# Kernel tuning notes

Hardware: AMD Instinct MI355X
Metric: run time of the kernel (lower is better)

## Reference

```python
import jax, jax.numpy as jnp
import numpy as np

B, T, D_IN, D_OUT, H = 4, 2048, 1024, 1024, 16
HD = D_OUT // H  # head_dim = 64


def setup_inputs() -> dict:
    key = jax.random.key(0)
    ks = jax.random.split(key, 6)
    s_in = 1.0 / np.sqrt(D_IN)
    s_out = 1.0 / np.sqrt(D_OUT)
    return {
        "x": jax.random.normal(ks[0], (B, T, D_IN), dtype=jnp.float32),
        "W_query": jax.random.uniform(ks[1], (D_IN, D_OUT), jnp.float32, -s_in, s_in),
        "W_key": jax.random.uniform(ks[2], (D_IN, D_OUT), jnp.float32, -s_in, s_in),
        "W_value": jax.random.uniform(ks[3], (D_IN, D_OUT), jnp.float32, -s_in, s_in),
        "W_out": jax.random.uniform(ks[4], (D_OUT, D_OUT), jnp.float32, -s_out, s_out),
        "b_out": jax.random.uniform(ks[5], (D_OUT,), jnp.float32, -s_out, s_out),
    }


def reference(x, W_query, W_key, W_value, W_out, b_out):
    # x: [B, T, D_IN]
    q = (x @ W_query).reshape(B, T, H, HD).transpose(0, 2, 1, 3)  # [B,H,T,HD]
    k = (x @ W_key).reshape(B, T, H, HD).transpose(0, 2, 1, 3)
    v = (x @ W_value).reshape(B, T, H, HD).transpose(0, 2, 1, 3)
    scores = jnp.einsum("bhqd,bhkd->bhqk", q, k)  # [B,H,T,T]
    causal = jnp.triu(jnp.ones((T, T), dtype=bool), k=1)
    scores = jnp.where(causal, -jnp.inf, scores)
    weights = jax.nn.softmax(scores / jnp.sqrt(jnp.float32(HD)), axis=-1)
    ctx = jnp.einsum("bhqk,bhkd->bhqd", weights, v)  # [B,H,T,HD]
    ctx = ctx.transpose(0, 2, 1, 3).reshape(B, T, D_OUT)
    return ctx @ W_out + b_out
```

## Files before the change

### kernel.cpp

```cpp
#include <hip/hip_runtime.h>
#include <math.h>

#define Bb   4
#define Tt   2048
#define DIN  1024
#define DOUT 1024
#define NH   16
#define HD   64
#define BT   (Bb * Tt)

typedef __attribute__((ext_vector_type(8))) short bf16x8;
typedef __attribute__((ext_vector_type(4))) float f32x4;
typedef __attribute__((ext_vector_type(4))) short short4v;

__device__ __forceinline__ short f2bf(float f) {
  union { float f; unsigned u; } v; v.f = f;
  unsigned r = v.u + 0x7FFFu + ((v.u >> 16) & 1u);
  return (short)(r >> 16);
}

__device__ __forceinline__ unsigned pkbf(float a, float b) {
  unsigned r;
  asm("v_cvt_pk_bf16_f32 %0, %1, %2" : "=v"(r) : "v"(a), "v"(b));
  return r;
}

#define MFMA16(a, b, c) __builtin_amdgcn_mfma_f32_16x16x32_bf16((a), (b), (c), 0, 0, 0)

__device__ __forceinline__ void gload16(const short* g, short* l) {
  __builtin_amdgcn_global_load_lds(
      (const __attribute__((address_space(1))) void*)g,
      (__attribute__((address_space(3))) void*)l, 16, 0, 0);
}

__global__ __launch_bounds__(256) void cvt_x(const float* __restrict__ x,
                                             short* __restrict__ xb) {
  const int i = (blockIdx.x * 256 + threadIdx.x) * 4;
  float4 v = *(const float4*)(x + i);
  uint2 o;
  o.x = pkbf(v.x, v.y);
  o.y = pkbf(v.z, v.w);
  *(uint2*)(xb + i) = o;
}

__global__ __launch_bounds__(256) void cvt_wt(
    const float* __restrict__ W0, const float* __restrict__ W1,
    const float* __restrict__ W2, const float* __restrict__ W3,
    short* __restrict__ O0, short* __restrict__ O1,
    short* __restrict__ O2, short* __restrict__ O3) {
  const float* W = blockIdx.z == 0 ? W0 : blockIdx.z == 1 ? W1
                 : blockIdx.z == 2 ? W2 : W3;
  short* O = blockIdx.z == 0 ? O0 : blockIdx.z == 1 ? O1
           : blockIdx.z == 2 ? O2 : O3;
  __shared__ short t[64][65];
  const int n0 = blockIdx.x * 64, k0 = blockIdx.y * 64;
  const int tid = threadIdx.x;
#pragma unroll
  for (int i = 0; i < 16; ++i) {
    const int e = tid + 256 * i;
    const int k = e >> 6, n = e & 63;
    t[n][k] = f2bf(W[(size_t)(k0 + k) * DOUT + n0 + n]);
  }
  __syncthreads();
#pragma unroll
  for (int i = 0; i < 16; ++i) {
    const int e = tid + 256 * i;
    const int n = e >> 6, k = e & 63;
    O[(size_t)(n0 + n) * DIN + k0 + k] = t[n][k];
  }
}

template <bool QKV, bool F32OUT, bool BIAS>
__global__ __launch_bounds__(256) void gemm_bf16(
    const short* __restrict__ A, const short* __restrict__ Bt0,
    const float* __restrict__ bias, void* __restrict__ Cout,
    int M, int N, int K, float qsc) {
  constexpr int BM = 128, BN = 128, BK = 64;
  __shared__ __align__(16) short Asm[BM][BK];
  __shared__ __align__(16) short Bsm[BN][BK];

  const short* Bt = Bt0;
  short* Cb16 = (short*)Cout;
  float oscale = 1.0f;
  if (QKV) {
    const int z = blockIdx.z;
    Bt += (size_t)z * N * K;
    Cb16 += (size_t)z * M * N;
    if (z == 0) oscale = qsc;
  }

  const int tid = threadIdx.x;
  const int wid = tid >> 6, lane = tid & 63;
  const int lhi = lane >> 4, llo = lane & 15;
  const int bm = blockIdx.x * BM, bn = blockIdx.y * BN;
  const int wr = (wid >> 1) * 64, wc = (wid & 1) * 64;

  const int srow = lane >> 3;
  const int sca = ((lane & 7) ^ srow) * 8;

  f32x4 acc[4][4];
#pragma unroll
  for (int i = 0; i < 4; ++i)
#pragma unroll
    for (int j = 0; j < 4; ++j)
#pragma unroll
      for (int r = 0; r < 4; ++r) acc[i][j][r] = 0.0f;

  for (int k0 = 0; k0 < K; k0 += BK) {
    __syncthreads();
#pragma unroll
    for (int iss = 0; iss < 4; ++iss) {
      const int ra = wid * 32 + iss * 8 + srow;
      gload16(A + (size_t)(bm + ra) * K + k0 + sca, &Asm[wid * 32 + iss * 8][0]);
      gload16(Bt + (size_t)(bn + ra) * K + k0 + sca, &Bsm[wid * 32 + iss * 8][0]);
    }
    __syncthreads();

#pragma unroll
    for (int ks = 0; ks < 2; ++ks) {
      bf16x8 af[4], bfr[4];
#pragma unroll
      for (int i = 0; i < 4; ++i) {
        const int row = wr + i * 16 + llo;
        af[i] = *(const bf16x8*)&Asm[row][((ks * 4 + lhi) ^ (row & 7)) * 8];
      }
#pragma unroll
      for (int j = 0; j < 4; ++j) {
        const int row = wc + j * 16 + llo;
        bfr[j] = *(const bf16x8*)&Bsm[row][((ks * 4 + lhi) ^ (row & 7)) * 8];
      }
      __builtin_amdgcn_s_setprio(1);
#pragma unroll
      for (int i = 0; i < 4; ++i)
#pragma unroll
        for (int j = 0; j < 4; ++j)
          acc[i][j] = MFMA16(af[i], bfr[j], acc[i][j]);
      __builtin_amdgcn_s_setprio(0);
    }
  }

#pragma unroll
  for (int i = 0; i < 4; ++i)
#pragma unroll
    for (int j = 0; j < 4; ++j)
#pragma unroll
      for (int r = 0; r < 4; ++r) {
        const int row = bm + wr + i * 16 + lhi * 4 + r;
        const int col = bn + wc + j * 16 + llo;
        float v = acc[i][j][r] * oscale;
        if (BIAS) v += bias[col];
        if (F32OUT)
          ((float*)Cout)[(size_t)row * N + col] = v;
        else
          Cb16[(size_t)row * N + col] = f2bf(v);
      }
}

__global__ __launch_bounds__(512, 2) void attn_bf16(
    const short* __restrict__ Q, const short* __restrict__ K,
    const short* __restrict__ Vt_g, short* __restrict__ Ctx) {
  constexpr int LDK = 72;
  constexpr int LDV = 72;
  constexpr int LDP = 72;
  __shared__ __align__(16) short Ks[2][64][LDK];
  __shared__ __align__(16) short Vt[2][64][LDV];
  __shared__ __align__(16) short Ps[8][32][LDP];

  const int bid = blockIdx.x;
  const int qt = 7 - (bid >> 6);
  const int bh = bid & 63;
  const int b = bh >> 4, h = bh & 15;
  const int tid = threadIdx.x;
  const int wid = tid >> 6, lane = tid & 63;
  const int lhi = lane >> 4, llo = lane & 15;

  const size_t base_bt = (size_t)b * Tt;
  const int headoff = h * HD;
  const int q0 = qt * 256 + wid * 32;

  bf16x8 qf[2][2];
#pragma unroll
  for (int rb = 0; rb < 2; ++rb)
#pragma unroll
    for (int kf = 0; kf < 2; ++kf)
      qf[rb][kf] = *(const bf16x8*)&Q[(base_bt + q0 + rb * 16 + llo) * DOUT +
                                      headoff + kf * 32 + lhi * 8];

  float m_r[2] = {-1e30f, -1e30f}, l_r[2] = {0.0f, 0.0f};
  f32x4 oa[2][4];
#pragma unroll
  for (int rb = 0; rb < 2; ++rb)
#pragma unroll
    for (int j = 0; j < 4; ++j)
#pragma unroll
      for (int r = 0; r < 4; ++r) oa[rb][j][r] = 0.0f;

  const int skv = tid >> 3;
  const int sd0 = (tid & 7) * 8;

  const int ktmax = qt * 4 + 3;

  const short* kgp = K + (base_bt + skv) * DOUT + headoff + sd0;
  const short* vgp = Vt_g + (size_t)(headoff + skv) * BT + base_bt + sd0;

  {
    bf16x8 kreg = *(const bf16x8*)kgp;
    bf16x8 vreg = *(const bf16x8*)vgp;
    *(bf16x8*)&Ks[0][skv][sd0] = kreg;
    *(bf16x8*)&Vt[0][skv][sd0] = vreg;
    kgp += 64 * DOUT;
    vgp += 64;
  }
  __syncthreads();

  for (int kt = 0; kt <= ktmax; ++kt) {
    const int cur = kt & 1;

    bf16x8 kreg, vreg;
    const bool haveNext = kt < ktmax;
    if (haveNext) {
      kreg = *(const bf16x8*)kgp;
      vreg = *(const bf16x8*)vgp;
      kgp += 64 * DOUT;
      vgp += 64;
    }

    if (kt * 64 <= q0 + 31) {
      bf16x8 kf0[4], kf1[4];
#pragma unroll
      for (int j = 0; j < 4; ++j) {
        kf0[j] = *(const bf16x8*)&Ks[cur][j * 16 + llo][lhi * 8];
        kf1[j] = *(const bf16x8*)&Ks[cur][j * 16 + llo][32 + lhi * 8];
      }

#pragma unroll
      for (int rb = 0; rb < 2; ++rb) {
        f32x4 s[4];
        __builtin_amdgcn_s_setprio(1);
#pragma unroll
        for (int j = 0; j < 4; ++j) {
#pragma unroll
          for (int r = 0; r < 4; ++r) s[j][r] = 0.0f;
          s[j] = MFMA16(kf0[j], qf[rb][0], s[j]);
          s[j] = MFMA16(kf1[j], qf[rb][1], s[j]);
        }
        __builtin_amdgcn_s_setprio(0);
        if (kt * 64 + 63 > q0 + rb * 16) {
          const int kvrel = kt * 64 + lhi * 4 - (q0 + rb * 16 + llo);
#pragma unroll
          for (int j = 0; j < 4; ++j)
#pragma unroll
            for (int r = 0; r < 4; ++r)
              if (kvrel + j * 16 + r > 0) s[j][r] = -1e30f;
        }
        float a0 = fmaxf(fmaxf(s[0][0], s[0][1]), fmaxf(s[0][2], s[0][3]));
        float a1 = fmaxf(fmaxf(s[1][0], s[1][1]), fmaxf(s[1][2], s[1][3]));
        float a2 = fmaxf(fmaxf(s[2][0], s[2][1]), fmaxf(s[2][2], s[2][3]));
        float a3 = fmaxf(fmaxf(s[3][0], s[3][1]), fmaxf(s[3][2], s[3][3]));
        float mx = fmaxf(fmaxf(a0, a1), fmaxf(a2, a3));
        mx = fmaxf(mx, __shfl_xor(mx, 16));
        mx = fmaxf(mx, __shfl_xor(mx, 32));
        if (!__all(mx - m_r[rb] <= 8.0f)) {
          const float mnew = fmaxf(m_r[rb], mx);
          const float al = exp2f(m_r[rb] - mnew);
          m_r[rb] = mnew;
          l_r[rb] *= al;
          float alr[4];
#pragma unroll
          for (int r = 0; r < 4; ++r) alr[r] = __shfl(al, (lhi << 2) | r, 16);
#pragma unroll
          for (int j = 0; j < 4; ++j)
#pragma unroll
            for (int r = 0; r < 4; ++r) oa[rb][j][r] *= alr[r];
        }
        const float mc = m_r[rb];
#pragma unroll
        for (int j = 0; j < 4; ++j)
#pragma unroll
          for (int r = 0; r < 4; ++r) s[j][r] = exp2f(s[j][r] - mc);
        float b0 = (s[0][0] + s[0][1]) + (s[0][2] + s[0][3]);
        float b1 = (s[1][0] + s[1][1]) + (s[1][2] + s[1][3]);
        float b2 = (s[2][0] + s[2][1]) + (s[2][2] + s[2][3]);
        float b3 = (s[3][0] + s[3][1]) + (s[3][2] + s[3][3]);
        float rs = (b0 + b1) + (b2 + b3);
        rs += __shfl_xor(rs, 16);
        rs += __shfl_xor(rs, 32);
        l_r[rb] += rs;
#pragma unroll
        for (int j = 0; j < 4; ++j) {
          uint2 w;
          w.x = pkbf(s[j][0], s[j][1]);
          w.y = pkbf(s[j][2], s[j][3]);
          *(uint2*)&Ps[wid][rb * 16 + llo][j * 16 + lhi * 4] = w;
        }
      }

      bf16x8 vfr[2][4];
#pragma unroll
      for (int ks = 0; ks < 2; ++ks)
#pragma unroll
        for (int j = 0; j < 4; ++j)
          vfr[ks][j] = *(const bf16x8*)&Vt[cur][j * 16 + llo][ks * 32 + lhi * 8];
      __builtin_amdgcn_s_setprio(1);
#pragma unroll
      for (int rb = 0; rb < 2; ++rb)
#pragma unroll
        for (int ks = 0; ks < 2; ++ks) {
          bf16x8 paf = *(const bf16x8*)&Ps[wid][rb * 16 + llo][lhi * 8 + ks * 32];
#pragma unroll
          for (int j = 0; j < 4; ++j)
            oa[rb][j] = MFMA16(paf, vfr[ks][j], oa[rb][j]);
        }
      __builtin_amdgcn_s_setprio(0);
    }

    if (haveNext) {
      const int nxt = cur ^ 1;
      *(bf16x8*)&Ks[nxt][skv][sd0] = kreg;
      *(bf16x8*)&Vt[nxt][skv][sd0] = vreg;
    }
    __syncthreads();
  }

#pragma unroll
  for (int rb = 0; rb < 2; ++rb) {
    const float linv = 1.0f / l_r[rb];
    float lr[4];
#pragma unroll
    for (int r = 0; r < 4; ++r) lr[r] = __shfl(linv, (lhi << 2) | r, 16);
#pragma unroll
    for (int j = 0; j < 4; ++j)
#pragma unroll
      for (int r = 0; r < 4; ++r) {
        const int row = q0 + rb * 16 + lhi * 4 + r;
        const int col = headoff + j * 16 + llo;
        Ctx[(base_bt + row) * DOUT + col] = f2bf(oa[rb][j][r] * lr[r]);
      }
  }
}

extern "C" void kernel_launch(void* const* d_in, const int* in_sizes, int n_in,
                              void* d_out, int out_size, void* d_ws, size_t ws_size,
                              hipStream_t stream) {
  const float* x  = (const float*)d_in[0];
  const float* Wq = (const float*)d_in[1];
  const float* Wk = (const float*)d_in[2];
  const float* Wv = (const float*)d_in[3];
  const float* Wo = (const float*)d_in[4];
  const float* bo = (const float*)d_in[5];
  float* out = (float*)d_out;

  const size_t NTD = (size_t)Bb * Tt * DOUT;
  const size_t WSZ = (size_t)DIN * DOUT;
  short* xb  = (short*)d_ws;
  short* Wqt = xb + NTD;
  short* Wkt = Wqt + WSZ;
  short* Wvt = Wkt + WSZ;
  short* Wot = Wvt + WSZ;
  short* Qb  = Wot + WSZ;
  short* Kb  = Qb + NTD;
  short* Vtb = Kb + NTD;
  short* Cb  = Vtb + NTD;

  const int M = Bb * Tt;
  const float qscale = 0.125f * 1.44269504089f;

  cvt_x<<<dim3(NTD / 1024), 256, 0, stream>>>(x, xb);
  cvt_wt<<<dim3(16, 16, 4), 256, 0, stream>>>(Wq, Wk, Wv, Wo, Wqt, Wkt, Wvt, Wot);

  gemm_bf16<true, false, false><<<dim3(64, 8, 2), 256, 0, stream>>>(
      xb, Wqt, nullptr, Qb, M, DOUT, DIN, qscale);
  gemm_bf16<false, false, false><<<dim3(8, 64), 256, 0, stream>>>(
      Wvt, xb, nullptr, Vtb, DOUT, M, DIN, 1.0f);

  attn_bf16<<<dim3(512), 512, 0, stream>>>(Qb, Kb, Vtb, Cb);

  gemm_bf16<false, true, true><<<dim3(64, 8), 256, 0, stream>>>(
      Cb, Wot, bo, out, M, DOUT, DOUT, 1.0f);
}
```

Baseline: 273.2 us.

## Keep P in registers via transposed PV MFMA and swizzled direct-to-LDS K/V loads

Reworks the attention kernel so the softmax probabilities stay in registers as MFMA B operands, using a permuted K row order and computing O transposed, which removes the per-wave P round trip through shared memory. K/V tiles are now loaded with direct global-to-LDS loads (gload16) into unpadded tiles that use an XOR swizzle instead of padding. This also removes the register staging and the rescale shuffles, and lets the output be stored as packed 4-element writes. It relies on the swizzle and permutation being correct and on gload16 existing in the unseen part of the file.

```diff
diff --git a/kernel.cpp b/kernel.cpp
--- a/kernel.cpp
+++ b/kernel.cpp
@@ -159,12 +159,8 @@
 __global__ __launch_bounds__(512, 2) void attn_bf16(
     const short* __restrict__ Q, const short* __restrict__ K,
     const short* __restrict__ Vt_g, short* __restrict__ Ctx) {
-  constexpr int LDK = 72;
-  constexpr int LDV = 72;
-  constexpr int LDP = 72;
-  __shared__ __align__(16) short Ks[2][64][LDK];
-  __shared__ __align__(16) short Vt[2][64][LDV];
-  __shared__ __align__(16) short Ps[8][32][LDP];
+  __shared__ __align__(16) short Ks[2][64][64];
+  __shared__ __align__(16) short Vt[2][64][64];
 
   const int bid = blockIdx.x;
   const int qt = 7 - (bid >> 6);
@@ -173,6 +169,7 @@
   const int tid = threadIdx.x;
   const int wid = tid >> 6, lane = tid & 63;
   const int lhi = lane >> 4, llo = lane & 15;
+  const int lm7 = llo & 7;
 
   const size_t base_bt = (size_t)b * Tt;
   const int headoff = h * HD;
@@ -182,77 +179,76 @@
 #pragma unroll
   for (int rb = 0; rb < 2; ++rb)
 #pragma unroll
-    for (int kf = 0; kf < 2; ++kf)
-      qf[rb][kf] = *(const bf16x8*)&Q[(base_bt + q0 + rb * 16 + llo) * DOUT +
-                                      headoff + kf * 32 + lhi * 8];
+    for (int kh = 0; kh < 2; ++kh)
+      qf[rb][kh] = *(const bf16x8*)&Q[(base_bt + q0 + rb * 16 + llo) * DOUT +
+                                      headoff + kh * 32 + lhi * 8];
 
   float m_r[2] = {-1e30f, -1e30f}, l_r[2] = {0.0f, 0.0f};
   f32x4 oa[2][4];
 #pragma unroll
   for (int rb = 0; rb < 2; ++rb)
 #pragma unroll
-    for (int j = 0; j < 4; ++j)
-#pragma unroll
-      for (int r = 0; r < 4; ++r) oa[rb][j][r] = 0.0f;
-
-  const int skv = tid >> 3;
-  const int sd0 = (tid & 7) * 8;
+    for (int d = 0; d < 4; ++d)
+#pragma unroll
+      for (int r = 0; r < 4; ++r) oa[rb][d][r] = 0.0f;
+
+  const int sm = tid >> 3, sc = tid & 7;
+  const int jg = sm >> 4, si = sm & 15;
+  const int pi = (jg >> 1) * 32 + (si >> 2) * 8 + (jg & 1) * 4 + (si & 3);
+  const int scs = (sc ^ (sm & 7)) * 8;
+
+  const short* kgp = K + (base_bt + pi) * DOUT + headoff + scs;
+  const short* vgp = Vt_g + (size_t)(headoff + sm) * BT + base_bt + scs;
+
+  const int klb0 = lhi * 8, klb1 = lhi * 8 + 4;
 
   const int ktmax = qt * 4 + 3;
 
-  const short* kgp = K + (base_bt + skv) * DOUT + headoff + sd0;
-  const short* vgp = Vt_g + (size_t)(headoff + skv) * BT + base_bt + sd0;
-
-  {
-    bf16x8 kreg = *(const bf16x8*)kgp;
-    bf16x8 vreg = *(const bf16x8*)vgp;
-    *(bf16x8*)&Ks[0][skv][sd0] = kreg;
-    *(bf16x8*)&Vt[0][skv][sd0] = vreg;
-    kgp += 64 * DOUT;
-    vgp += 64;
-  }
+  gload16(kgp, &Ks[0][wid * 8][0]);
+  gload16(vgp, &Vt[0][wid * 8][0]);
+  kgp += 64 * DOUT;
+  vgp += 64;
   __syncthreads();
 
   for (int kt = 0; kt <= ktmax; ++kt) {
-    const int cur = kt & 1;
-
-    bf16x8 kreg, vreg;
-    const bool haveNext = kt < ktmax;
-    if (haveNext) {
-      kreg = *(const bf16x8*)kgp;
-      vreg = *(const bf16x8*)vgp;
+    const int cur = kt & 1, nxt = cur ^ 1;
+
+    if (kt < ktmax) {
+      gload16(kgp, &Ks[nxt][wid * 8][0]);
+      gload16(vgp, &Vt[nxt][wid * 8][0]);
       kgp += 64 * DOUT;
       vgp += 64;
     }
 
     if (kt * 64 <= q0 + 31) {
-      bf16x8 kf0[4], kf1[4];
-#pragma unroll
-      for (int j = 0; j < 4; ++j) {
-        kf0[j] = *(const bf16x8*)&Ks[cur][j * 16 + llo][lhi * 8];
-        kf1[j] = *(const bf16x8*)&Ks[cur][j * 16 + llo][32 + lhi * 8];
-      }
-
+      bf16x8 pb[2][2];
 #pragma unroll
       for (int rb = 0; rb < 2; ++rb) {
         f32x4 s[4];
         __builtin_amdgcn_s_setprio(1);
 #pragma unroll
         for (int j = 0; j < 4; ++j) {
+          const int row = j * 16 + llo;
+          bf16x8 kfa = *(const bf16x8*)&Ks[cur][row][(lhi ^ lm7) * 8];
+          bf16x8 kfb = *(const bf16x8*)&Ks[cur][row][((4 + lhi) ^ lm7) * 8];
 #pragma unroll
           for (int r = 0; r < 4; ++r) s[j][r] = 0.0f;
-          s[j] = MFMA16(kf0[j], qf[rb][0], s[j]);
-          s[j] = MFMA16(kf1[j], qf[rb][1], s[j]);
+          s[j] = MFMA16(kfa, qf[rb][0], s[j]);
+          s[j] = MFMA16(kfb, qf[rb][1], s[j]);
         }
         __builtin_amdgcn_s_setprio(0);
+
         if (kt * 64 + 63 > q0 + rb * 16) {
-          const int kvrel = kt * 64 + lhi * 4 - (q0 + rb * 16 + llo);
-#pragma unroll
-          for (int j = 0; j < 4; ++j)
+          const int qrel = q0 + rb * 16 + llo - kt * 64;
+#pragma unroll
+          for (int j = 0; j < 4; ++j) {
+            const int kb = (j >> 1) * 32 + ((j & 1) ? klb1 : klb0);
 #pragma unroll
             for (int r = 0; r < 4; ++r)
-              if (kvrel + j * 16 + r > 0) s[j][r] = -1e30f;
-        }
+              if (kb + r > qrel) s[j][r] = -1e30f;
+          }
+        }
+
         float a0 = fmaxf(fmaxf(s[0][0], s[0][1]), fmaxf(s[0][2], s[0][3]));
         float a1 = fmaxf(fmaxf(s[1][0], s[1][1]), fmaxf(s[1][2], s[1][3]));
         float a2 = fmaxf(fmaxf(s[2][0], s[2][1]), fmaxf(s[2][2], s[2][3]));
@@ -260,18 +256,16 @@
         float mx = fmaxf(fmaxf(a0, a1), fmaxf(a2, a3));
         mx = fmaxf(mx, __shfl_xor(mx, 16));
         mx = fmaxf(mx, __shfl_xor(mx, 32));
+
         if (!__all(mx - m_r[rb] <= 8.0f)) {
           const float mnew = fmaxf(m_r[rb], mx);
           const float al = exp2f(m_r[rb] - mnew);
           m_r[rb] = mnew;
           l_r[rb] *= al;
-          float alr[4];
-#pragma unroll
-          for (int r = 0; r < 4; ++r) alr[r] = __shfl(al, (lhi << 2) | r, 16);
-#pragma unroll
-          for (int j = 0; j < 4; ++j)
-#pragma unroll
-            for (int r = 0; r < 4; ++r) oa[rb][j][r] *= alr[r];
+#pragma unroll
+          for (int d = 0; d < 4; ++d)
+#pragma unroll
+            for (int r = 0; r < 4; ++r) oa[rb][d][r] *= al;
         }
         const float mc = m_r[rb];
 #pragma unroll
@@ -286,56 +280,46 @@
         rs += __shfl_xor(rs, 16);
         rs += __shfl_xor(rs, 32);
         l_r[rb] += rs;
-#pragma unroll
-        for (int j = 0; j < 4; ++j) {
-          uint2 w;
-          w.x = pkbf(s[j][0], s[j][1]);
-          w.y = pkbf(s[j][2], s[j][3]);
-          *(uint2*)&Ps[wid][rb * 16 + llo][j * 16 + lhi * 4] = w;
-        }
-      }
-
-      bf16x8 vfr[2][4];
-#pragma unroll
-      for (int ks = 0; ks < 2; ++ks)
-#pragma unroll
-        for (int j = 0; j < 4; ++j)
-          vfr[ks][j] = *(const bf16x8*)&Vt[cur][j * 16 + llo][ks * 32 + lhi * 8];
-      __builtin_amdgcn_s_setprio(1);
-#pragma unroll
-      for (int rb = 0; rb < 2; ++rb)
-#pragma unroll
-        for (int ks = 0; ks < 2; ++ks) {
-          bf16x8 paf = *(const bf16x8*)&Ps[wid][rb * 16 + llo][lhi * 8 + ks * 32];
-#pragma unroll
-          for (int j = 0; j < 4; ++j)
-            oa[rb][j] = MFMA16(paf, vfr[ks][j], oa[rb][j]);
-        }
-      __builtin_amdgcn_s_setprio(0);
-    }
-
-    if (haveNext) {
-      const int nxt = cur ^ 1;
-      *(bf16x8*)&Ks[nxt][skv][sd0] = kreg;
-      *(bf16x8*)&Vt[nxt][skv][sd0] = vreg;
-    }
+
+#pragma unroll
+        for (int jj = 0; jj < 2; ++jj) {
+          union { bf16x8 v; unsigned u[4]; } w;
+          w.u[0] = pkbf(s[2 * jj][0], s[2 * jj][1]);
+          w.u[1] = pkbf(s[2 * jj][2], s[2 * jj][3]);
+          w.u[2] = pkbf(s[2 * jj + 1][0], s[2 * jj + 1][1]);
+          w.u[3] = pkbf(s[2 * jj + 1][2], s[2 * jj + 1][3]);
+          pb[rb][jj] = w.v;
+        }
+      }
+
+#pragma unroll
+      for (int d = 0; d < 4; ++d) {
+        __builtin_amdgcn_s_setprio(1);
+#pragma unroll
+        for (int jj = 0; jj < 2; ++jj) {
+          bf16x8 vfr = *(const bf16x8*)
+              &Vt[cur][d * 16 + llo][((jj * 4 + lhi) ^ lm7) * 8];
+          oa[0][d] = MFMA16(vfr, pb[0][jj], oa[0][d]);
+          oa[1][d] = MFMA16(vfr, pb[1][jj], oa[1][d]);
+        }
+        __builtin_amdgcn_s_setprio(0);
+      }
+    }
+
     __syncthreads();
   }
 
 #pragma unroll
   for (int rb = 0; rb < 2; ++rb) {
-    const float linv = 1.0f / l_r[rb];
-    float lr[4];
-#pragma unroll
-    for (int r = 0; r < 4; ++r) lr[r] = __shfl(linv, (lhi << 2) | r, 16);
-#pragma unroll
-    for (int j = 0; j < 4; ++j)
-#pragma unroll
-      for (int r = 0; r < 4; ++r) {
-        const int row = q0 + rb * 16 + lhi * 4 + r;
-        const int col = headoff + j * 16 + llo;
-        Ctx[(base_bt + row) * DOUT + col] = f2bf(oa[rb][j][r] * lr[r]);
-      }
+    const float li = 1.0f / l_r[rb];
+    const size_t rowoff = (base_bt + q0 + rb * 16 + llo) * DOUT + headoff;
+#pragma unroll
+    for (int d = 0; d < 4; ++d) {
+      uint2 w;
+      w.x = pkbf(oa[rb][d][0] * li, oa[rb][d][1] * li);
+      w.y = pkbf(oa[rb][d][2] * li, oa[rb][d][3] * li);
+      *(uint2*)&Ctx[rowoff + d * 16 + lhi * 4] = w;
+    }
   }
 }
 
```

After: 274.2 us. About the same (+0.4%).
